# Kernel tuning notes

Measured on AMD Instinct MI355X. Metric: run time of the kernel, lower is better.

The kernel has to match this reference:

```python
import jax, jax.numpy as jnp
import numpy as np

EPS = 1e-4
MAX_LAPLACE_VAR = 1000.0
MAX_DENSITY = 10000.0
BINS = 256

_LAP_KERNEL = jnp.array([[0., 1., 0.], [1., -4., 1.], [0., 1., 0.]], dtype=jnp.float32)[None, None]  # OIHW [1,1,3,3]


def setup_inputs() -> dict:
    key = jax.random.key(0)
    k1, k2 = jax.random.split(key)
    rgb_img = jax.random.uniform(k1, (32, 3, 512, 512), dtype=jnp.float32)
    depth_img = jax.random.normal(k2, (32, 1, 512, 512), dtype=jnp.float32)
    return {"rgb_img": rgb_img, "depth_img": depth_img}


def _rgb_confidence(rgb_img):
    B, C, H, W = rgb_img.shape
    gray = 0.299 * rgb_img[:, 0] + 0.587 * rgb_img[:, 1] + 0.114 * rgb_img[:, 2]  # [B,H,W]
    gray = gray[:, None]  # [B,1,H,W]
    lap = jax.lax.conv_general_dilated(
        gray, _LAP_KERNEL, window_strides=(1, 1), padding=[(1, 1), (1, 1)],
        dimension_numbers=("NCHW", "OIHW", "NCHW"))
    # torch.var default is unbiased (ddof=1)
    laplace_var = jnp.var(lap, axis=(1, 2, 3), ddof=1)

    # integer-valued pixels 0..255 land exactly in histc bins 0..255 (bins=256, min=0, max=255)
    vals = jnp.clip(gray * 255.0, 0.0, 255.0).astype(jnp.int32)  # [B,1,H,W]
    vals = vals.reshape(B, -1)  # [B, H*W]
    bidx = jnp.broadcast_to(jnp.arange(B)[:, None], vals.shape)
    hist = jnp.zeros((B, BINS), jnp.float32).at[bidx, vals].add(1.0)
    p = hist / jnp.sum(hist, axis=1, keepdims=True)
    entropy = -jnp.sum(p * jnp.log2(p + EPS), axis=1)

    clarity_score = laplace_var / (MAX_LAPLACE_VAR + EPS)
    uniformity_score = 1.0 / (entropy + EPS)
    return (0.5 * (clarity_score + uniformity_score))[:, None]  # [B,1]


def _depth_confidence(depth_img):
    C = depth_img.shape[1]
    depth_map = depth_img[:, 2] if C == 3 else depth_img[:, 0]  # [B,H,W]
    mask = (depth_map > 0).astype(jnp.float32)
    density = jnp.mean(mask, axis=(1, 2))

    # vectorized masked std (unbiased, ddof=1), matching torch.std over valid pixels
    n = jnp.sum(mask, axis=(1, 2))  # [B]
    mean = jnp.sum(depth_map * mask, axis=(1, 2)) / jnp.maximum(n, 1.0)
    sq = jnp.sum(mask * (depth_map - mean[:, None, None]) ** 2, axis=(1, 2))
    var = sq / jnp.maximum(n - 1.0, 1.0)
    std = jnp.sqrt(jnp.maximum(var, 0.0))
    noise_level = jnp.where(n > 0, std, 1.0)

    density_score = density / (MAX_DENSITY + EPS)
    noise_score = 1.0 / (noise_level + EPS)
    return (0.5 * (density_score + noise_score))[:, None]  # [B,1]


def reference(rgb_img, depth_img):
    rgb_conf = _rgb_confidence(rgb_img)
    depth_conf = _depth_confidence(depth_img)
    denom = rgb_conf + depth_conf + EPS
    w_r = rgb_conf / denom
    w_d = depth_conf / denom
    return (w_r, w_d)
```

## Files before the change

### kernel.cpp

```cpp
#include <hip/hip_runtime.h>

#define IMG_H 512
#define IMG_W 512
#define HW (IMG_H * IMG_W)
#define NB 32
#define STRIPS 16
#define RPW 8

#define ACC_DOUBLES 160
#define WS_BYTES (ACC_DOUBLES * 8 + NB * 256 * 4)

__device__ inline void load_gray(const float* __restrict__ rp, int r, int lane,
                                 float g[8]) {
    if ((unsigned)r < IMG_H) {
        const size_t o = (size_t)r * IMG_W + 4 * lane;
        const float4 rA = *(const float4*)(rp + o);
        const float4 rB = *(const float4*)(rp + o + 256);
        const float4 gA = *(const float4*)(rp + HW + o);
        const float4 gB = *(const float4*)(rp + HW + o + 256);
        const float4 bA = *(const float4*)(rp + 2 * HW + o);
        const float4 bB = *(const float4*)(rp + 2 * HW + o + 256);
        g[0] = 0.299f * rA.x + 0.587f * gA.x + 0.114f * bA.x;
        g[1] = 0.299f * rA.y + 0.587f * gA.y + 0.114f * bA.y;
        g[2] = 0.299f * rA.z + 0.587f * gA.z + 0.114f * bA.z;
        g[3] = 0.299f * rA.w + 0.587f * gA.w + 0.114f * bA.w;
        g[4] = 0.299f * rB.x + 0.587f * gB.x + 0.114f * bB.x;
        g[5] = 0.299f * rB.y + 0.587f * gB.y + 0.114f * bB.y;
        g[6] = 0.299f * rB.z + 0.587f * gB.z + 0.114f * bB.z;
        g[7] = 0.299f * rB.w + 0.587f * gB.w + 0.114f * bB.w;
    } else {
        #pragma unroll
        for (int j = 0; j < 8; ++j) g[j] = 0.f;
    }
}

__global__ __launch_bounds__(256, 2) void fused_kernel(
    const float* __restrict__ rgb, const float* __restrict__ depth,
    double* __restrict__ acc, unsigned int* __restrict__ hist)
{
    __shared__ unsigned int lh[4][256];
    __shared__ double red[4][5];

    const int t = threadIdx.x;
    const int b = blockIdx.y;
    const int s = blockIdx.x;
    const int lane = t & 63;
    const int w = t >> 6;

    #pragma unroll
    for (int i = 0; i < 4; ++i) lh[i][t & 255] = 0u;
    __syncthreads();

    const float* rp = rgb + (size_t)b * 3 * HW;
    const int rb = s * 32 + w * RPW;

    const float4* dpw = (const float4*)(depth + (size_t)b * HW
                                        + (size_t)s * (HW / STRIPS)) + w * 1024;

    float gp[8], gc[8], gn[8];
    load_gray(rp, rb - 1, lane, gp);
    load_gray(rp, rb, lane, gc);

    float s1 = 0.f, s2 = 0.f;
    float dnf = 0.f, dsf = 0.f, dqf = 0.f;

    #pragma unroll
    for (int r = 0; r < RPW; ++r) {
        load_gray(rp, rb + r + 1, lane, gn);
        const float4 d0 = dpw[r * 128 + lane];
        const float4 d1 = dpw[r * 128 + 64 + lane];

        float lA = __shfl_up(gc[3], 1, 64);
        if (lane == 0) lA = 0.f;
        float rA = __shfl_down(gc[0], 1, 64);
        const float seamR = __shfl(gc[4], 0, 64);
        if (lane == 63) rA = seamR;
        float lB = __shfl_up(gc[7], 1, 64);
        const float seamL = __shfl(gc[3], 63, 64);
        if (lane == 0) lB = seamL;
        float rB = __shfl_down(gc[4], 1, 64);
        if (lane == 63) rB = 0.f;

        #pragma unroll
        for (int j = 0; j < 8; ++j) {
            float left, right;
            if (j == 0)      { left = lA;        right = gc[1]; }
            else if (j == 3) { left = gc[2];     right = rA; }
            else if (j == 4) { left = lB;        right = gc[5]; }
            else if (j == 7) { left = gc[6];     right = rB; }
            else             { left = gc[j - 1]; right = gc[j + 1]; }
            const float lap = gp[j] + gn[j] + left + right - 4.f * gc[j];
            s1 += lap;
            s2 += lap * lap;
            atomicAdd(&lh[w][(int)fminf(fmaxf(gc[j] * 255.f, 0.f), 255.f)], 1u);
        }

        if (d0.x > 0.f) { dnf += 1.f; dsf += d0.x; dqf += d0.x * d0.x; }
        if (d0.y > 0.f) { dnf += 1.f; dsf += d0.y; dqf += d0.y * d0.y; }
        if (d0.z > 0.f) { dnf += 1.f; dsf += d0.z; dqf += d0.z * d0.z; }
        if (d0.w > 0.f) { dnf += 1.f; dsf += d0.w; dqf += d0.w * d0.w; }
        if (d1.x > 0.f) { dnf += 1.f; dsf += d1.x; dqf += d1.x * d1.x; }
        if (d1.y > 0.f) { dnf += 1.f; dsf += d1.y; dqf += d1.y * d1.y; }
        if (d1.z > 0.f) { dnf += 1.f; dsf += d1.z; dqf += d1.z * d1.z; }
        if (d1.w > 0.f) { dnf += 1.f; dsf += d1.w; dqf += d1.w * d1.w; }

        #pragma unroll
        for (int j = 0; j < 8; ++j) { gp[j] = gc[j]; gc[j] = gn[j]; }
    }

    double z0 = (double)s1, z1 = (double)s2, z2 = (double)dnf, z3 = (double)dsf, z4 = (double)dqf;
    for (int off = 32; off > 0; off >>= 1) {
        z0 += __shfl_down(z0, off, 64);
        z1 += __shfl_down(z1, off, 64);
        z2 += __shfl_down(z2, off, 64);
        z3 += __shfl_down(z3, off, 64);
        z4 += __shfl_down(z4, off, 64);
    }
    if (lane == 0) {
        red[w][0] = z0; red[w][1] = z1; red[w][2] = z2; red[w][3] = z3; red[w][4] = z4;
    }
    __syncthreads();

    const unsigned int hsum = lh[0][t] + lh[1][t] + lh[2][t] + lh[3][t];
    atomicAdd(&hist[b * 256 + t], hsum);
    if (t < 5) {
        const double v = red[0][t] + red[1][t] + red[2][t] + red[3][t];
        atomicAdd(&acc[t * 32 + b], v);
    }
}

__global__ __launch_bounds__(256) void final_kernel(
    const double* __restrict__ acc,
    const unsigned int* __restrict__ hist,
    float* __restrict__ out)
{
    __shared__ float part[256];
    const int t = threadIdx.x;
    const int b = t >> 3;
    const int sl = t & 7;
    float e = 0.f;
    #pragma unroll
    for (int i = 0; i < 32; ++i) {
        const float p = (float)hist[b * 256 + sl * 32 + i] * (1.0f / (float)HW);
        e += p * log2f(p + 1e-4f);
    }
    part[t] = e;
    __syncthreads();

    if (t < NB) {
        float es = 0.f;
        #pragma unroll
        for (int i = 0; i < 8; ++i) es += part[t * 8 + i];
        const double entropy = -(double)es;
        const double N = (double)HW;

        const double ls = acc[t], lq = acc[32 + t];
        const double lvar = (lq - ls * ls / N) / (N - 1.0);
        const double clarity = lvar / (1000.0 + 1e-4);
        const double uniformity = 1.0 / (entropy + 1e-4);
        const double rgb_conf = 0.5 * (clarity + uniformity);

        const double n = acc[64 + t], sdep = acc[96 + t], q = acc[128 + t];
        const double mean = sdep / fmax(n, 1.0);
        const double sq = q - 2.0 * mean * sdep + mean * mean * n;
        const double var = sq / fmax(n - 1.0, 1.0);
        const double stdd = sqrt(fmax(var, 0.0));
        const double noise = (n > 0.0) ? stdd : 1.0;
        const double density = n / N;
        const double depth_conf = 0.5 * (density / (10000.0 + 1e-4) + 1.0 / (noise + 1e-4));

        const double denom = rgb_conf + depth_conf + 1e-4;
        out[t]      = (float)(rgb_conf / denom);
        out[NB + t] = (float)(depth_conf / denom);
    }
}

extern "C" void kernel_launch(void* const* d_in, const int* in_sizes, int n_in,
                              void* d_out, int out_size, void* d_ws, size_t ws_size,
                              hipStream_t stream) {
    const float* rgb   = (const float*)d_in[0];
    const float* depth = (const float*)d_in[1];
    float* out = (float*)d_out;

    double* acc = (double*)d_ws;
    unsigned int* hist = (unsigned int*)((char*)d_ws + ACC_DOUBLES * 8);

    hipMemsetAsync(d_ws, 0, WS_BYTES, stream);

    fused_kernel<<<dim3(STRIPS, NB), 256, 0, stream>>>(rgb, depth, acc, hist);
    final_kernel<<<1, 256, 0, stream>>>(acc, hist, out);
}
```

Baseline: 181.3 us.

## Split fused kernel into gray/hist/depth pass and separate Laplacian pass

Replaces the single fused kernel with two passes. The first computes grayscale, the histogram and the depth statistics, and writes the gray image to workspace. The second reads the gray image and computes Laplacian sums, loading each strip's rows with a halo. This removes the repeated RGB loads and gray recomputation for halo rows and lets both kernels run at higher occupancy. The cost is an extra 32 MB gray write and read plus one more kernel launch.

New measurement: 188.4 us. +3.9%, slower.

```diff
diff --git a/kernel.cpp b/kernel.cpp
--- a/kernel.cpp
+++ b/kernel.cpp
@@ -4,42 +4,82 @@
 #define IMG_W 512
 #define HW (IMG_H * IMG_W)
 #define NB 32
-#define STRIPS 16
-#define RPW 8
 
 #define ACC_DOUBLES 160
-#define WS_BYTES (ACC_DOUBLES * 8 + NB * 256 * 4)
-
-__device__ inline void load_gray(const float* __restrict__ rp, int r, int lane,
-                                 float g[8]) {
-    if ((unsigned)r < IMG_H) {
-        const size_t o = (size_t)r * IMG_W + 4 * lane;
-        const float4 rA = *(const float4*)(rp + o);
-        const float4 rB = *(const float4*)(rp + o + 256);
-        const float4 gA = *(const float4*)(rp + HW + o);
-        const float4 gB = *(const float4*)(rp + HW + o + 256);
-        const float4 bA = *(const float4*)(rp + 2 * HW + o);
-        const float4 bB = *(const float4*)(rp + 2 * HW + o + 256);
-        g[0] = 0.299f * rA.x + 0.587f * gA.x + 0.114f * bA.x;
-        g[1] = 0.299f * rA.y + 0.587f * gA.y + 0.114f * bA.y;
-        g[2] = 0.299f * rA.z + 0.587f * gA.z + 0.114f * bA.z;
-        g[3] = 0.299f * rA.w + 0.587f * gA.w + 0.114f * bA.w;
-        g[4] = 0.299f * rB.x + 0.587f * gB.x + 0.114f * bB.x;
-        g[5] = 0.299f * rB.y + 0.587f * gB.y + 0.114f * bB.y;
-        g[6] = 0.299f * rB.z + 0.587f * gB.z + 0.114f * bB.z;
-        g[7] = 0.299f * rB.w + 0.587f * gB.w + 0.114f * bB.w;
-    } else {
-        #pragma unroll
-        for (int j = 0; j < 8; ++j) g[j] = 0.f;
-    }
-}
-
-__global__ __launch_bounds__(256, 2) void fused_kernel(
+#define ZERO_BYTES (ACC_DOUBLES * 8 + NB * 256 * 4)
+#define GRAY_OFF 65536
+
+__global__ __launch_bounds__(256, 4) void gray_hist_depth_kernel(
     const float* __restrict__ rgb, const float* __restrict__ depth,
-    double* __restrict__ acc, unsigned int* __restrict__ hist)
+    float* __restrict__ gray, double* __restrict__ acc,
+    unsigned int* __restrict__ hist)
 {
     __shared__ unsigned int lh[4][256];
-    __shared__ double red[4][5];
+    __shared__ double red[4][3];
+
+    const int t = threadIdx.x;
+    const int b = blockIdx.y;
+    const int x = blockIdx.x;
+    const int lane = t & 63;
+    const int w = t >> 6;
+
+    #pragma unroll
+    for (int i = 0; i < 4; ++i) lh[i][t] = 0u;
+    __syncthreads();
+
+    const float4* rp = (const float4*)(rgb + (size_t)b * 3 * HW);
+    const float4* gp = rp + (HW / 4);
+    const float4* bp = rp + 2 * (HW / 4);
+    const float4* dp = (const float4*)(depth + (size_t)b * HW);
+    float4* gw = (float4*)(gray + (size_t)b * HW);
+
+    const int base = x * 1024 + t;
+    float dnf = 0.f, dsf = 0.f, dqf = 0.f;
+
+    #pragma unroll
+    for (int i = 0; i < 4; ++i) {
+        const int idx = base + i * 256;
+        const float4 r4 = rp[idx];
+        const float4 g4 = gp[idx];
+        const float4 b4 = bp[idx];
+        const float4 d4 = dp[idx];
+        float4 g;
+        g.x = 0.299f * r4.x + 0.587f * g4.x + 0.114f * b4.x;
+        g.y = 0.299f * r4.y + 0.587f * g4.y + 0.114f * b4.y;
+        g.z = 0.299f * r4.z + 0.587f * g4.z + 0.114f * b4.z;
+        g.w = 0.299f * r4.w + 0.587f * g4.w + 0.114f * b4.w;
+        gw[idx] = g;
+        atomicAdd(&lh[w][(int)fminf(fmaxf(g.x * 255.f, 0.f), 255.f)], 1u);
+        atomicAdd(&lh[w][(int)fminf(fmaxf(g.y * 255.f, 0.f), 255.f)], 1u);
+        atomicAdd(&lh[w][(int)fminf(fmaxf(g.z * 255.f, 0.f), 255.f)], 1u);
+        atomicAdd(&lh[w][(int)fminf(fmaxf(g.w * 255.f, 0.f), 255.f)], 1u);
+        if (d4.x > 0.f) { dnf += 1.f; dsf += d4.x; dqf += d4.x * d4.x; }
+        if (d4.y > 0.f) { dnf += 1.f; dsf += d4.y; dqf += d4.y * d4.y; }
+        if (d4.z > 0.f) { dnf += 1.f; dsf += d4.z; dqf += d4.z * d4.z; }
+        if (d4.w > 0.f) { dnf += 1.f; dsf += d4.w; dqf += d4.w * d4.w; }
+    }
+
+    double z2 = (double)dnf, z3 = (double)dsf, z4 = (double)dqf;
+    for (int off = 32; off > 0; off >>= 1) {
+        z2 += __shfl_down(z2, off, 64);
+        z3 += __shfl_down(z3, off, 64);
+        z4 += __shfl_down(z4, off, 64);
+    }
+    if (lane == 0) { red[w][0] = z2; red[w][1] = z3; red[w][2] = z4; }
+    __syncthreads();
+
+    const unsigned int hsum = lh[0][t] + lh[1][t] + lh[2][t] + lh[3][t];
+    atomicAdd(&hist[b * 256 + t], hsum);
+    if (t < 3) {
+        const double v = red[0][t] + red[1][t] + red[2][t] + red[3][t];
+        atomicAdd(&acc[64 + t * 32 + b], v);
+    }
+}
+
+__global__ __launch_bounds__(256, 4) void lap_kernel(
+    const float* __restrict__ gray, double* __restrict__ acc)
+{
+    __shared__ double red[4][2];
 
     const int t = threadIdx.x;
     const int b = blockIdx.y;
@@ -47,28 +87,31 @@
     const int lane = t & 63;
     const int w = t >> 6;
 
-    #pragma unroll
-    for (int i = 0; i < 4; ++i) lh[i][t & 255] = 0u;
-    __syncthreads();
-
-    const float* rp = rgb + (size_t)b * 3 * HW;
-    const int rb = s * 32 + w * RPW;
-
-    const float4* dpw = (const float4*)(depth + (size_t)b * HW
-                                        + (size_t)s * (HW / STRIPS)) + w * 1024;
-
-    float gp[8], gc[8], gn[8];
-    load_gray(rp, rb - 1, lane, gp);
-    load_gray(rp, rb, lane, gc);
+    const float* gp = gray + (size_t)b * HW;
+    const int rb = s * 16 + w * 4;
+
+    float gr[6][8];
+    #pragma unroll
+    for (int k = 0; k < 6; ++k) {
+        const int r = rb - 1 + k;
+        if ((unsigned)r < IMG_H) {
+            const size_t o = (size_t)r * IMG_W + 4 * lane;
+            const float4 a = *(const float4*)(gp + o);
+            const float4 c = *(const float4*)(gp + o + 256);
+            gr[k][0] = a.x; gr[k][1] = a.y; gr[k][2] = a.z; gr[k][3] = a.w;
+            gr[k][4] = c.x; gr[k][5] = c.y; gr[k][6] = c.z; gr[k][7] = c.w;
+        } else {
+            #pragma unroll
+            for (int j = 0; j < 8; ++j) gr[k][j] = 0.f;
+        }
+    }
 
     float s1 = 0.f, s2 = 0.f;
-    float dnf = 0.f, dsf = 0.f, dqf = 0.f;
-
-    #pragma unroll
-    for (int r = 0; r < RPW; ++r) {
-        load_gray(rp, rb + r + 1, lane, gn);
-        const float4 d0 = dpw[r * 128 + lane];
-        const float4 d1 = dpw[r * 128 + 64 + lane];
+    #pragma unroll
+    for (int j = 0; j < 4; ++j) {
+        const float* up = gr[j];
+        const float* gc = gr[j + 1];
+        const float* dn = gr[j + 2];
 
         float lA = __shfl_up(gc[3], 1, 64);
         if (lane == 0) lA = 0.f;
@@ -82,48 +125,27 @@
         if (lane == 63) rB = 0.f;
 
         #pragma unroll
-        for (int j = 0; j < 8; ++j) {
+        for (int k = 0; k < 8; ++k) {
             float left, right;
-            if (j == 0)      { left = lA;        right = gc[1]; }
-            else if (j == 3) { left = gc[2];     right = rA; }
-            else if (j == 4) { left = lB;        right = gc[5]; }
-            else if (j == 7) { left = gc[6];     right = rB; }
-            else             { left = gc[j - 1]; right = gc[j + 1]; }
-            const float lap = gp[j] + gn[j] + left + right - 4.f * gc[j];
+            if (k == 0)      { left = lA;        right = gc[1]; }
+            else if (k == 3) { left = gc[2];     right = rA; }
+            else if (k == 4) { left = lB;        right = gc[5]; }
+            else if (k == 7) { left = gc[6];     right = rB; }
+            else             { left = gc[k - 1]; right = gc[k + 1]; }
+            const float lap = up[k] + dn[k] + left + right - 4.f * gc[k];
             s1 += lap;
             s2 += lap * lap;
-            atomicAdd(&lh[w][(int)fminf(fmaxf(gc[j] * 255.f, 0.f), 255.f)], 1u);
         }
-
-        if (d0.x > 0.f) { dnf += 1.f; dsf += d0.x; dqf += d0.x * d0.x; }
-        if (d0.y > 0.f) { dnf += 1.f; dsf += d0.y; dqf += d0.y * d0.y; }
-        if (d0.z > 0.f) { dnf += 1.f; dsf += d0.z; dqf += d0.z * d0.z; }
-        if (d0.w > 0.f) { dnf += 1.f; dsf += d0.w; dqf += d0.w * d0.w; }
-        if (d1.x > 0.f) { dnf += 1.f; dsf += d1.x; dqf += d1.x * d1.x; }
-        if (d1.y > 0.f) { dnf += 1.f; dsf += d1.y; dqf += d1.y * d1.y; }
-        if (d1.z > 0.f) { dnf += 1.f; dsf += d1.z; dqf += d1.z * d1.z; }
-        if (d1.w > 0.f) { dnf += 1.f; dsf += d1.w; dqf += d1.w * d1.w; }
-
-        #pragma unroll
-        for (int j = 0; j < 8; ++j) { gp[j] = gc[j]; gc[j] = gn[j]; }
-    }
-
-    double z0 = (double)s1, z1 = (double)s2, z2 = (double)dnf, z3 = (double)dsf, z4 = (double)dqf;
+    }
+
+    double z0 = (double)s1, z1 = (double)s2;
     for (int off = 32; off > 0; off >>= 1) {
         z0 += __shfl_down(z0, off, 64);
         z1 += __shfl_down(z1, off, 64);
-        z2 += __shfl_down(z2, off, 64);
-        z3 += __shfl_down(z3, off, 64);
-        z4 += __shfl_down(z4, off, 64);
-    }
-    if (lane == 0) {
-        red[w][0] = z0; red[w][1] = z1; red[w][2] = z2; red[w][3] = z3; red[w][4] = z4;
-    }
-    __syncthreads();
-
-    const unsigned int hsum = lh[0][t] + lh[1][t] + lh[2][t] + lh[3][t];
-    atomicAdd(&hist[b * 256 + t], hsum);
-    if (t < 5) {
+    }
+    if (lane == 0) { red[w][0] = z0; red[w][1] = z1; }
+    __syncthreads();
+    if (t < 2) {
         const double v = red[0][t] + red[1][t] + red[2][t] + red[3][t];
         atomicAdd(&acc[t * 32 + b], v);
     }
@@ -184,9 +206,11 @@
 
     double* acc = (double*)d_ws;
     unsigned int* hist = (unsigned int*)((char*)d_ws + ACC_DOUBLES * 8);
-
-    hipMemsetAsync(d_ws, 0, WS_BYTES, stream);
-
-    fused_kernel<<<dim3(STRIPS, NB), 256, 0, stream>>>(rgb, depth, acc, hist);
+    float* gray = (float*)((char*)d_ws + GRAY_OFF);
+
+    hipMemsetAsync(d_ws, 0, ZERO_BYTES, stream);
+
+    gray_hist_depth_kernel<<<dim3(64, NB), 256, 0, stream>>>(rgb, depth, gray, acc, hist);
+    lap_kernel<<<dim3(32, NB), 256, 0, stream>>>(gray, acc);
     final_kernel<<<1, 256, 0, stream>>>(acc, hist, out);
 }
```
